# Optimization experiments

Hardware: AMD Instinct MI355X
Metric: run time of the kernel (lower is better)

Reference implementation:

```python
import jax, jax.numpy as jnp
import numpy as np

N_NODES = 50000
N_EDGES = 800000
IN_DIM = 256
HIDDEN = 64
HEADS1 = 4
HEADS2 = 1
N_CLASSES = 64
NEG_SLOPE = 0.2


def setup_inputs() -> dict:
    key = jax.random.key(0)
    ks = jax.random.split(key, 12)
    x = jax.random.normal(ks[0], (N_NODES, IN_DIM), dtype=jnp.float32)
    src = jax.random.randint(ks[1], (N_EDGES,), 0, N_NODES, dtype=jnp.int32)
    dst = jax.random.randint(ks[2], (N_EDGES,), 0, N_NODES, dtype=jnp.int32)
    s1 = 1.0 / np.sqrt(IN_DIM)
    s2 = 1.0 / np.sqrt(HIDDEN * HEADS1)
    W1 = jax.random.normal(ks[3], (IN_DIM, HEADS1 * HIDDEN), dtype=jnp.float32) * s1
    aL1 = jax.random.normal(ks[4], (HEADS1, HIDDEN), dtype=jnp.float32) * 0.1
    aR1 = jax.random.normal(ks[5], (HEADS1, HIDDEN), dtype=jnp.float32) * 0.1
    b1 = jnp.zeros((HEADS1 * HIDDEN,), dtype=jnp.float32)
    W2 = jax.random.normal(ks[6], (HEADS1 * HIDDEN, HEADS2 * N_CLASSES), dtype=jnp.float32) * s2
    aL2 = jax.random.normal(ks[7], (HEADS2, N_CLASSES), dtype=jnp.float32) * 0.1
    aR2 = jax.random.normal(ks[8], (HEADS2, N_CLASSES), dtype=jnp.float32) * 0.1
    b2 = jnp.zeros((HEADS2 * N_CLASSES,), dtype=jnp.float32)
    resW2 = jax.random.normal(ks[9], (HEADS1 * HIDDEN, HEADS2 * N_CLASSES), dtype=jnp.float32) * s2
    return {"x": x, "W1": W1, "aL1": aL1, "aR1": aR1, "b1": b1,
            "W2": W2, "aL2": aL2, "aR2": aR2, "b2": b2, "resW2": resW2,
            "src": src, "dst": dst}


def _gat_layer(h, W, aL, aR, b, src, dst, heads, out_dim, res_W=None, activation=None):
    n = h.shape[0]
    feat = (h @ W).reshape(n, heads, out_dim)          # [N, H, D]
    el = jnp.sum(feat * aL, axis=-1)                    # [N, H]
    er = jnp.sum(feat * aR, axis=-1)                    # [N, H]
    e = el[src] + er[dst]                               # [E, H]
    e = jnp.where(e > 0, e, NEG_SLOPE * e)              # leaky_relu
    # edge softmax over incoming edges of each destination node
    m = jax.ops.segment_max(e, dst, num_segments=n)
    ex = jnp.exp(e - m[dst])
    s = jax.ops.segment_sum(ex, dst, num_segments=n)
    sd = s[dst]
    a = ex / jnp.where(sd > 0, sd, 1.0)                 # [E, H]
    msg = feat[src] * a[:, :, None]                     # [E, H, D]
    rst = jax.ops.segment_sum(msg, dst, num_segments=n)  # [N, H, D]
    if res_W is not None:
        rst = rst + (h @ res_W).reshape(n, heads, out_dim)
    rst = rst + b.reshape(1, heads, out_dim)
    if activation is not None:
        rst = activation(rst)
    return rst


def reference(x, W1, aL1, aR1, b1, W2, aL2, aR2, b2, resW2, src, dst):
    h = _gat_layer(x, W1, aL1, aR1, b1, src, dst, HEADS1, HIDDEN,
                   res_W=None, activation=jax.nn.elu)
    h = h.reshape(N_NODES, HEADS1 * HIDDEN)             # flatten(1)
    h = _gat_layer(h, W2, aL2, aR2, b2, src, dst, HEADS2, N_CLASSES,
                   res_W=resW2, activation=None)
    return h.mean(axis=1)                               # mean over heads
```

## Files before the change

### kernel.cpp

```cpp
#include <hip/hip_runtime.h>
#include <hip/hip_bf16.h>
#include <math.h>

#define N_NODES 50000
#define N_EDGES 800000
#define IN_DIM  256
#define HID     64
#define H1      4
#define F1      256
#define NC      64
#define CHUNK   128
#define NB_SCAN 49

typedef __attribute__((ext_vector_type(8))) short short8v;
typedef __attribute__((ext_vector_type(4))) float float4v;

__device__ __forceinline__ float bf2f(unsigned short u){
  union { unsigned int i; float f; } c; c.i = ((unsigned int)u) << 16; return c.f;
}


__global__ __launch_bounds__(256) void prep_kernel(int* __restrict__ counts,
                                                   const float* __restrict__ W1,
                                                   const float* __restrict__ W2,
                                                   const float* __restrict__ resW2,
                                                   __hip_bfloat16* __restrict__ W1T,
                                                   __hip_bfloat16* __restrict__ B2T){
  int i = blockIdx.x*256 + threadIdx.x;
  if (i < N_NODES) counts[i] = 0;
  if (i < 256*256){
    int n = i >> 8, k = i & 255;
    W1T[n*256 + k] = __float2bfloat16(W1[k*256 + n]);
  }
  if (i < 128*256){
    int n = i >> 8, k = i & 255;
    float v = (n < 64) ? W2[k*64 + n] : resW2[k*64 + (n - 64)];
    B2T[n*256 + k] = __float2bfloat16(v);
  }
}


__global__ void hist_kernel(const int* __restrict__ dst, int* __restrict__ counts, int E4){
  int e4 = blockIdx.x*256 + threadIdx.x;
  if (e4 < E4){
    int4 d = ((const int4*)dst)[e4];
    atomicAdd(&counts[d.x], 1);
    atomicAdd(&counts[d.y], 1);
    atomicAdd(&counts[d.z], 1);
    atomicAdd(&counts[d.w], 1);
  }
}

__global__ __launch_bounds__(1024) void scan1_kernel(const int* __restrict__ counts,
                                                     int* __restrict__ part,
                                                     int* __restrict__ bsum, int n){
  __shared__ int wsum[16];
  int b = blockIdx.x, tid = threadIdx.x;
  int i = b*1024 + tid;
  int lane = tid & 63, wid = tid >> 6;
  int x = (i < n) ? counts[i] : 0;
  #pragma unroll
  for (int off = 1; off < 64; off <<= 1){ int t = __shfl_up(x, off); if (lane >= off) x += t; }
  if (lane == 63) wsum[wid] = x;
  __syncthreads();
  if (wid == 0 && lane < 16){
    int w = wsum[lane];
    #pragma unroll
    for (int off = 1; off < 16; off <<= 1){ int t = __shfl_up(w, off); if (lane >= off) w += t; }
    wsum[lane] = w;
  }
  __syncthreads();
  int incl = x + (wid ? wsum[wid-1] : 0);
  if (i < n) part[i] = incl;
  if (tid == 1023) bsum[b] = incl;
}

__global__ __launch_bounds__(1024) void scan3_kernel(const int* __restrict__ part,
                                                     const int* __restrict__ bsum,
                                                     int* __restrict__ row_ptr,
                                                     int* __restrict__ cursor, int n){
  __shared__ int off_s;
  int b = blockIdx.x, tid = threadIdx.x;
  if (tid < 64){
    int orig = (tid < NB_SCAN) ? bsum[tid] : 0;
    int x = orig;
    #pragma unroll
    for (int o = 1; o < 64; o <<= 1){ int t = __shfl_up(x, o); if (tid >= o) x += t; }
    if (tid == b) off_s = x - orig;
  }
  __syncthreads();
  int i = b*1024 + tid;
  if (i < n){
    int v = part[i] + off_s;
    row_ptr[i+1] = v; cursor[i+1] = v;
  }
  if (i == 0){ row_ptr[0] = 0; cursor[0] = 0; }
}

__global__ void fill_kernel(const int* __restrict__ src, const int* __restrict__ dst,
                            int* __restrict__ cursor, int* __restrict__ csr_src, int E){
  int e = blockIdx.x*256 + threadIdx.x;
  if (e < E){
    int slot = atomicAdd(&cursor[dst[e]], 1);
    csr_src[slot] = src[e];
  }
}


template<int LAYER, bool AFP32>
__device__ __forceinline__ void gemm_body(
    const void* __restrict__ Araw,
    const __hip_bfloat16* __restrict__ BT,
    __hip_bfloat16* __restrict__ Fb,
    float* __restrict__ Res,
    float* __restrict__ el, float* __restrict__ er,
    const float* __restrict__ aL, const float* __restrict__ aR,
    int M, int bm, int bn)
{
  constexpr int K = 256;
  __shared__ __hip_bfloat16 As[128*72];
  __shared__ __hip_bfloat16 Bs[128*72];
  int tid = threadIdx.x;
  int lane = tid & 63, w = tid >> 6;
  int wr = w >> 1, wc = w & 1;
  int l15 = lane & 15, l4 = lane >> 4;

  float4v acc[4][4];
  #pragma unroll
  for (int i=0;i<4;i++)
    #pragma unroll
    for (int j=0;j<4;j++) acc[i][j] = (float4v){0.f,0.f,0.f,0.f};

  for (int kt = 0; kt < K; kt += 64){
    #pragma unroll
    for (int it = 0; it < 4; it++){
      int chunk = tid + it*256;
      int r = chunk >> 3, kc = (chunk & 7)*8;
      int arow = bm*128 + r;
      if (AFP32){
        const float* Af = (const float*)Araw;
        float4 v0 = make_float4(0,0,0,0), v1 = make_float4(0,0,0,0);
        if (arow < M){
          v0 = *(const float4*)&Af[(size_t)arow*K + kt + kc];
          v1 = *(const float4*)&Af[(size_t)arow*K + kt + kc + 4];
        }
        __hip_bfloat16 t[8] = {__float2bfloat16(v0.x),__float2bfloat16(v0.y),
                               __float2bfloat16(v0.z),__float2bfloat16(v0.w),
                               __float2bfloat16(v1.x),__float2bfloat16(v1.y),
                               __float2bfloat16(v1.z),__float2bfloat16(v1.w)};
        *(int4*)&As[r*72 + kc] = *(int4*)t;
      } else {
        const __hip_bfloat16* Ab = (const __hip_bfloat16*)Araw;
        int4 va = make_int4(0,0,0,0);
        if (arow < M) va = *(const int4*)&Ab[(size_t)arow*K + kt + kc];
        *(int4*)&As[r*72 + kc] = va;
      }
      int brow = bn*128 + r;
      int4 vb = *(const int4*)&BT[(size_t)brow*K + kt + kc];
      *(int4*)&Bs[r*72 + kc] = vb;
    }
    __syncthreads();
    short8v af[4][2], bfr[4][2];
    #pragma unroll
    for (int mi=0;mi<4;mi++)
      #pragma unroll
      for (int kf=0;kf<2;kf++)
        af[mi][kf] = *(const short8v*)&As[(wr*64 + mi*16 + l15)*72 + kf*32 + l4*8];
    #pragma unroll
    for (int ni=0;ni<4;ni++)
      #pragma unroll
      for (int kf=0;kf<2;kf++)
        bfr[ni][kf] = *(const short8v*)&Bs[(wc*64 + ni*16 + l15)*72 + kf*32 + l4*8];
    #pragma unroll
    for (int mi=0;mi<4;mi++)
      #pragma unroll
      for (int ni=0;ni<4;ni++){
        acc[mi][ni] = __builtin_amdgcn_mfma_f32_16x16x32_bf16(af[mi][0], bfr[ni][0], acc[mi][ni], 0,0,0);
        acc[mi][ni] = __builtin_amdgcn_mfma_f32_16x16x32_bf16(af[mi][1], bfr[ni][1], acc[mi][ni], 0,0,0);
      }
    __syncthreads();
  }

  if (LAYER == 1){
    int h = bn*2 + wc;
    float aLv[4], aRv[4];
    #pragma unroll
    for (int ni=0;ni<4;ni++){ aLv[ni] = aL[h*64 + ni*16 + l15]; aRv[ni] = aR[h*64 + ni*16 + l15]; }
    #pragma unroll
    for (int mi=0;mi<4;mi++){
      #pragma unroll
      for (int r=0;r<4;r++){
        int row = bm*128 + wr*64 + mi*16 + l4*4 + r;
        float sl = 0.f, sr = 0.f;
        #pragma unroll
        for (int ni=0;ni<4;ni++){ float v = acc[mi][ni][r]; sl += v*aLv[ni]; sr += v*aRv[ni]; }
        #pragma unroll
        for (int off=1; off<16; off<<=1){ sl += __shfl_xor(sl, off); sr += __shfl_xor(sr, off); }
        if (row < M){
          #pragma unroll
          for (int ni=0;ni<4;ni++)
            Fb[(size_t)row*256 + h*64 + ni*16 + l15] = __float2bfloat16(acc[mi][ni][r]);
          if (l15 == 0){ el[row*4 + h] = sl; er[row*4 + h] = sr; }
        }
      }
    }
  } else {
    if (wc == 0){
      float aLv[4], aRv[4];
      #pragma unroll
      for (int ni=0;ni<4;ni++){ aLv[ni] = aL[ni*16 + l15]; aRv[ni] = aR[ni*16 + l15]; }
      #pragma unroll
      for (int mi=0;mi<4;mi++){
        #pragma unroll
        for (int r=0;r<4;r++){
          int row = bm*128 + wr*64 + mi*16 + l4*4 + r;
          float sl = 0.f, sr = 0.f;
          #pragma unroll
          for (int ni=0;ni<4;ni++){ float v = acc[mi][ni][r]; sl += v*aLv[ni]; sr += v*aRv[ni]; }
          #pragma unroll
          for (int off=1; off<16; off<<=1){ sl += __shfl_xor(sl, off); sr += __shfl_xor(sr, off); }
          if (row < M){
            #pragma unroll
            for (int ni=0;ni<4;ni++)
              Fb[(size_t)row*64 + ni*16 + l15] = __float2bfloat16(acc[mi][ni][r]);
            if (l15 == 0){ el[row] = sl; er[row] = sr; }
          }
        }
      }
    } else {
      #pragma unroll
      for (int mi=0;mi<4;mi++){
        #pragma unroll
        for (int r=0;r<4;r++){
          int row = bm*128 + wr*64 + mi*16 + l4*4 + r;
          if (row < M){
            #pragma unroll
            for (int ni=0;ni<4;ni++)
              Res[(size_t)row*64 + ni*16 + l15] = acc[mi][ni][r];
          }
        }
      }
    }
  }
}

__global__ __launch_bounds__(256) void gemm1_kernel(
    const float* __restrict__ x, const __hip_bfloat16* __restrict__ W1T,
    __hip_bfloat16* __restrict__ featb,
    float* __restrict__ el, float* __restrict__ er,
    const float* __restrict__ aL, const float* __restrict__ aR)
{
  int id = blockIdx.x;
  int bn = (id >> 3) & 1;
  int bm = (id & 7) | ((id >> 4) << 3);
  if (bm*128 >= N_NODES) return;
  gemm_body<1,true>(x, W1T, featb, nullptr, el, er, aL, aR, N_NODES, bm, bn);
}

__global__ __launch_bounds__(256) void gemm2_kernel(
    const __hip_bfloat16* __restrict__ A, const __hip_bfloat16* __restrict__ BT,
    __hip_bfloat16* __restrict__ Fb, float* __restrict__ Res,
    float* __restrict__ el, float* __restrict__ er,
    const float* __restrict__ aL, const float* __restrict__ aR, int M)
{
  gemm_body<2,false>(A, BT, Fb, Res, el, er, aL, aR, M, blockIdx.x, 0);
}


__global__ __launch_bounds__(256) void agg1_kernel(const int* __restrict__ row_ptr,
                                                   const int* __restrict__ csr_src,
                                                   const float* __restrict__ el,
                                                   const float* __restrict__ er,
                                                   const __hip_bfloat16* __restrict__ featb,
                                                   const float* __restrict__ bias,
                                                   __hip_bfloat16* __restrict__ h1b, int N){
  __shared__ int   ssh[4][CHUNK];
  __shared__ float wsh[4][CHUNK][4];
  int lane = threadIdx.x & 63, wv = threadIdx.x >> 6;
  int n = blockIdx.x*4 + wv;
  if (n >= N) return;
  int rs = row_ptr[n], re = row_ptr[n+1];
  int half = lane >> 5;
  int l31 = lane & 31;
  int hl = l31 >> 3;
  float4 ern4 = *(const float4*)&er[(size_t)n*4];
  float ernv[4] = {ern4.x, ern4.y, ern4.z, ern4.w};
  float acc[8] = {0.f,0.f,0.f,0.f,0.f,0.f,0.f,0.f};
  float ssum4[4] = {0.f,0.f,0.f,0.f};

  for (int base = rs; base < re; base += CHUNK){
    int cnt = min(CHUNK, re - base);
    int padded = (cnt + 7) & ~7;
    for (int t = lane; t < padded; t += 64){
      float w4[4] = {0.f,0.f,0.f,0.f};
      int s = 0;
      if (t < cnt){
        s = csr_src[base + t];
        float4 e4 = *(const float4*)&el[(size_t)s*4];
        float ev[4] = {e4.x, e4.y, e4.z, e4.w};
        #pragma unroll
        for (int h = 0; h < 4; h++){
          float e = ev[h] + ernv[h];
          e = e > 0.f ? e : 0.2f*e;
          float ex = __expf(e);
          w4[h] = ex;
          ssum4[h] += ex;
        }
      }
      ssh[wv][t] = s;
      *(float4*)&wsh[wv][t][0] = make_float4(w4[0], w4[1], w4[2], w4[3]);
    }
    for (int jb = 0; jb < padded; jb += 8){
      int t0 = jb + half, t1 = jb + 2 + half, t2 = jb + 4 + half, t3 = jb + 6 + half;
      int s0 = ssh[wv][t0], s1 = ssh[wv][t1], s2 = ssh[wv][t2], s3 = ssh[wv][t3];
      float w0 = wsh[wv][t0][hl], w1 = wsh[wv][t1][hl];
      float w2 = wsh[wv][t2][hl], w3 = wsh[wv][t3][hl];
      short8v f0 = *(const short8v*)&featb[(size_t)s0*256 + l31*8];
      short8v f1 = *(const short8v*)&featb[(size_t)s1*256 + l31*8];
      short8v f2 = *(const short8v*)&featb[(size_t)s2*256 + l31*8];
      short8v f3 = *(const short8v*)&featb[(size_t)s3*256 + l31*8];
      #pragma unroll
      for (int q = 0; q < 8; q++){
        acc[q] += w0 * bf2f((unsigned short)f0[q]);
        acc[q] += w1 * bf2f((unsigned short)f1[q]);
        acc[q] += w2 * bf2f((unsigned short)f2[q]);
        acc[q] += w3 * bf2f((unsigned short)f3[q]);
      }
    }
  }
  #pragma unroll
  for (int off = 32; off; off >>= 1)
    #pragma unroll
    for (int h = 0; h < 4; h++) ssum4[h] += __shfl_xor(ssum4[h], off);
  #pragma unroll
  for (int q = 0; q < 8; q++) acc[q] += __shfl_xor(acc[q], 32);
  float inv = ssum4[hl] > 0.f ? 1.f/ssum4[hl] : 0.f;
  if (lane < 32){
    float4 b0 = *(const float4*)&bias[l31*8];
    float4 b1v = *(const float4*)&bias[l31*8 + 4];
    float bb[8] = {b0.x,b0.y,b0.z,b0.w,b1v.x,b1v.y,b1v.z,b1v.w};
    __hip_bfloat16 o[8];
    #pragma unroll
    for (int q = 0; q < 8; q++){
      float v = acc[q]*inv + bb[q];
      v = v > 0.f ? v : __expf(v) - 1.f;
      o[q] = __float2bfloat16(v);
    }
    *(short8v*)&h1b[(size_t)n*256 + l31*8] = *(short8v*)o;
  }
}

__global__ __launch_bounds__(256) void agg2_kernel(const int* __restrict__ row_ptr,
                                                   const int* __restrict__ csr_src,
                                                   const float* __restrict__ el,
                                                   const float* __restrict__ er,
                                                   const __hip_bfloat16* __restrict__ f2b,
                                                   const float* __restrict__ res,
                                                   const float* __restrict__ bias,
                                                   float* __restrict__ out, int N){
  __shared__ int   ssh[4][CHUNK];
  __shared__ float wsh[4][CHUNK];
  int lane = threadIdx.x & 63, wv = threadIdx.x >> 6;
  int n = blockIdx.x*4 + wv;
  if (n >= N) return;
  int rs = row_ptr[n], re = row_ptr[n+1];
  int q4 = lane >> 4;
  int l15 = lane & 15;
  float ern = er[n];
  float acc[4] = {0.f,0.f,0.f,0.f};
  float ssum = 0.f;

  for (int base = rs; base < re; base += CHUNK){
    int cnt = min(CHUNK, re - base);
    int padded = (cnt + 15) & ~15;
    for (int t = lane; t < padded; t += 64){
      float w = 0.f; int s = 0;
      if (t < cnt){
        s = csr_src[base + t];
        float e = el[s] + ern;
        e = e > 0.f ? e : 0.2f*e;
        w = __expf(e);
        ssum += w;
      }
      ssh[wv][t] = s;
      wsh[wv][t] = w;
    }
    for (int jb = 0; jb < padded; jb += 16){
      int t0 = jb + q4, t1 = jb + 4 + q4, t2 = jb + 8 + q4, t3 = jb + 12 + q4;
      int s0 = ssh[wv][t0], s1 = ssh[wv][t1], s2 = ssh[wv][t2], s3 = ssh[wv][t3];
      float w0 = wsh[wv][t0], w1 = wsh[wv][t1], w2 = wsh[wv][t2], w3 = wsh[wv][t3];
      ushort4 f0 = *(const ushort4*)&f2b[(size_t)s0*NC + l15*4];
      ushort4 f1 = *(const ushort4*)&f2b[(size_t)s1*NC + l15*4];
      ushort4 f2 = *(const ushort4*)&f2b[(size_t)s2*NC + l15*4];
      ushort4 f3 = *(const ushort4*)&f2b[(size_t)s3*NC + l15*4];
      acc[0] += w0*bf2f(f0.x) + w1*bf2f(f1.x) + w2*bf2f(f2.x) + w3*bf2f(f3.x);
      acc[1] += w0*bf2f(f0.y) + w1*bf2f(f1.y) + w2*bf2f(f2.y) + w3*bf2f(f3.y);
      acc[2] += w0*bf2f(f0.z) + w1*bf2f(f1.z) + w2*bf2f(f2.z) + w3*bf2f(f3.z);
      acc[3] += w0*bf2f(f0.w) + w1*bf2f(f1.w) + w2*bf2f(f2.w) + w3*bf2f(f3.w);
    }
  }
  #pragma unroll
  for (int off = 32; off; off >>= 1) ssum += __shfl_xor(ssum, off);
  #pragma unroll
  for (int q = 0; q < 4; q++){
    acc[q] += __shfl_xor(acc[q], 16);
    acc[q] += __shfl_xor(acc[q], 32);
  }
  float inv = ssum > 0.f ? 1.f/ssum : 0.f;
  if (lane < 16){
    float4 r4 = *(const float4*)&res[(size_t)n*NC + l15*4];
    float4 b4 = *(const float4*)&bias[l15*4];
    float4 o;
    o.x = acc[0]*inv + r4.x + b4.x;
    o.y = acc[1]*inv + r4.y + b4.y;
    o.z = acc[2]*inv + r4.z + b4.z;
    o.w = acc[3]*inv + r4.w + b4.w;
    *(float4*)&out[(size_t)n*NC + l15*4] = o;
  }
}


extern "C" void kernel_launch(void* const* d_in, const int* in_sizes, int n_in,
                              void* d_out, int out_size, void* d_ws, size_t ws_size,
                              hipStream_t stream){
  const float* x     = (const float*)d_in[0];
  const float* W1    = (const float*)d_in[1];
  const float* aL1   = (const float*)d_in[2];
  const float* aR1   = (const float*)d_in[3];
  const float* b1    = (const float*)d_in[4];
  const float* W2    = (const float*)d_in[5];
  const float* aL2   = (const float*)d_in[6];
  const float* aR2   = (const float*)d_in[7];
  const float* b2    = (const float*)d_in[8];
  const float* resW2 = (const float*)d_in[9];
  const int*   src   = (const int*)d_in[10];
  const int*   dst   = (const int*)d_in[11];
  float* out = (float*)d_out;

  char* p = (char*)d_ws;
  auto alloc = [&](size_t bytes)->void*{
    void* r = (void*)p; p += (bytes + 255) & ~(size_t)255; return r;
  };
  __hip_bfloat16* featb = (__hip_bfloat16*)alloc((size_t)N_NODES*F1*2);
  __hip_bfloat16* h1b   = (__hip_bfloat16*)alloc((size_t)N_NODES*F1*2);
  __hip_bfloat16* f2b   = (__hip_bfloat16*)alloc((size_t)N_NODES*NC*2);
  float* res   = (float*)alloc((size_t)N_NODES*NC*4);
  float* el1   = (float*)alloc((size_t)N_NODES*H1*4);
  float* er1   = (float*)alloc((size_t)N_NODES*H1*4);
  float* el2   = (float*)alloc((size_t)N_NODES*4);
  float* er2   = (float*)alloc((size_t)N_NODES*4);
  int* counts  = (int*)alloc((size_t)N_NODES*4);
  int* part    = (int*)alloc((size_t)N_NODES*4);
  int* bsum    = (int*)alloc((size_t)64*4);
  int* row_ptr = (int*)alloc((size_t)(N_NODES+1)*4);
  int* cursor  = (int*)alloc((size_t)(N_NODES+1)*4);
  int* csr_src = (int*)alloc((size_t)N_EDGES*4);
  __hip_bfloat16* W1T = (__hip_bfloat16*)alloc((size_t)256*256*2);
  __hip_bfloat16* B2T = (__hip_bfloat16*)alloc((size_t)128*256*2);

  int nb = (N_NODES + 1023)/1024;
  prep_kernel<<<256, 256, 0, stream>>>(counts, W1, W2, resW2, W1T, B2T);
  hist_kernel<<<(N_EDGES/4+255)/256, 256, 0, stream>>>(dst, counts, N_EDGES/4);
  scan1_kernel<<<nb, 1024, 0, stream>>>(counts, part, bsum, N_NODES);
  scan3_kernel<<<nb, 1024, 0, stream>>>(part, bsum, row_ptr, cursor, N_NODES);
  fill_kernel<<<(N_EDGES+255)/256, 256, 0, stream>>>(src, dst, cursor, csr_src, N_EDGES);

  gemm1_kernel<<<800, 256, 0, stream>>>(x, W1T, featb, el1, er1, aL1, aR1);
  agg1_kernel<<<(N_NODES+3)/4, 256, 0, stream>>>(row_ptr, csr_src, el1, er1, featb, b1, h1b, N_NODES);

  gemm2_kernel<<<(N_NODES+127)/128, 256, 0, stream>>>(h1b, B2T, f2b, res,
                                                      el2, er2, aL2, aR2, N_NODES);
  agg2_kernel<<<(N_NODES+3)/4, 256, 0, stream>>>(row_ptr, csr_src, el2, er2, f2b, res, b2, out, N_NODES);
}
```

Before: 234.5 us.

## Fuse CSR fill into gemm1 launch and histogram into weight prep kernel

Merges independent kernels by splitting the block range of a single launch: the dst histogram shares a launch with the weight transpose and cast, and the CSR fill shares a launch with the layer-1 GEMM. Zeroing of counts moves to a memset. The aim is fewer launches and letting the atomic-bound fill overlap with the compute-bound GEMM on otherwise idle CUs. In exchange, the fill blocks contend with GEMM blocks for memory bandwidth and scheduling slots, and the added memset is an extra queued operation.

```diff
diff --git a/kernel.cpp b/kernel.cpp
--- a/kernel.cpp
+++ b/kernel.cpp
@@ -11,6 +11,9 @@
 #define NC      64
 #define CHUNK   128
 #define NB_SCAN 49
+#define GEMM1_BLOCKS 800
+#define FILL_BLOCKS  ((N_EDGES+255)/256)
+#define HIST4_BLOCKS ((N_EDGES/4+255)/256)
 
 typedef __attribute__((ext_vector_type(8))) short short8v;
 typedef __attribute__((ext_vector_type(4))) float float4v;
@@ -20,36 +23,35 @@
 }
 
 
-__global__ __launch_bounds__(256) void prep_kernel(int* __restrict__ counts,
-                                                   const float* __restrict__ W1,
-                                                   const float* __restrict__ W2,
-                                                   const float* __restrict__ resW2,
-                                                   __hip_bfloat16* __restrict__ W1T,
-                                                   __hip_bfloat16* __restrict__ B2T){
-  int i = blockIdx.x*256 + threadIdx.x;
-  if (i < N_NODES) counts[i] = 0;
-  if (i < 256*256){
-    int n = i >> 8, k = i & 255;
-    W1T[n*256 + k] = __float2bfloat16(W1[k*256 + n]);
-  }
-  if (i < 128*256){
-    int n = i >> 8, k = i & 255;
-    float v = (n < 64) ? W2[k*64 + n] : resW2[k*64 + (n - 64)];
-    B2T[n*256 + k] = __float2bfloat16(v);
-  }
-}
-
-
-__global__ void hist_kernel(const int* __restrict__ dst, int* __restrict__ counts, int E4){
-  int e4 = blockIdx.x*256 + threadIdx.x;
-  if (e4 < E4){
-    int4 d = ((const int4*)dst)[e4];
-    atomicAdd(&counts[d.x], 1);
-    atomicAdd(&counts[d.y], 1);
-    atomicAdd(&counts[d.z], 1);
-    atomicAdd(&counts[d.w], 1);
-  }
-}
+__global__ __launch_bounds__(256) void hist_prepw_kernel(
+    const int* __restrict__ dst, int* __restrict__ counts,
+    const float* __restrict__ W1, const float* __restrict__ W2,
+    const float* __restrict__ resW2,
+    __hip_bfloat16* __restrict__ W1T, __hip_bfloat16* __restrict__ B2T){
+  int b = blockIdx.x;
+  if (b < HIST4_BLOCKS){
+    int e4 = b*256 + threadIdx.x;
+    if (e4 < N_EDGES/4){
+      int4 d = ((const int4*)dst)[e4];
+      atomicAdd(&counts[d.x], 1);
+      atomicAdd(&counts[d.y], 1);
+      atomicAdd(&counts[d.z], 1);
+      atomicAdd(&counts[d.w], 1);
+    }
+  } else {
+    int i = (b - HIST4_BLOCKS)*256 + threadIdx.x;
+    if (i < 256*256){
+      int n = i >> 8, k = i & 255;
+      W1T[n*256 + k] = __float2bfloat16(W1[k*256 + n]);
+    } else if (i < 256*256 + 128*256){
+      int j = i - 256*256;
+      int n = j >> 8, k = j & 255;
+      float v = (n < 64) ? W2[k*64 + n] : resW2[k*64 + (n - 64)];
+      B2T[n*256 + k] = __float2bfloat16(v);
+    }
+  }
+}
+
 
 __global__ __launch_bounds__(1024) void scan1_kernel(const int* __restrict__ counts,
                                                      int* __restrict__ part,
@@ -95,15 +97,6 @@
     row_ptr[i+1] = v; cursor[i+1] = v;
   }
   if (i == 0){ row_ptr[0] = 0; cursor[0] = 0; }
-}
-
-__global__ void fill_kernel(const int* __restrict__ src, const int* __restrict__ dst,
-                            int* __restrict__ cursor, int* __restrict__ csr_src, int E){
-  int e = blockIdx.x*256 + threadIdx.x;
-  if (e < E){
-    int slot = atomicAdd(&cursor[dst[e]], 1);
-    csr_src[slot] = src[e];
-  }
 }
 
 
@@ -244,17 +237,27 @@
   }
 }
 
-__global__ __launch_bounds__(256) void gemm1_kernel(
+__global__ __launch_bounds__(256) void gemm1_fill_kernel(
     const float* __restrict__ x, const __hip_bfloat16* __restrict__ W1T,
     __hip_bfloat16* __restrict__ featb,
     float* __restrict__ el, float* __restrict__ er,
-    const float* __restrict__ aL, const float* __restrict__ aR)
+    const float* __restrict__ aL, const float* __restrict__ aR,
+    const int* __restrict__ src, const int* __restrict__ dst,
+    int* __restrict__ cursor, int* __restrict__ csr_src)
 {
   int id = blockIdx.x;
-  int bn = (id >> 3) & 1;
-  int bm = (id & 7) | ((id >> 4) << 3);
-  if (bm*128 >= N_NODES) return;
-  gemm_body<1,true>(x, W1T, featb, nullptr, el, er, aL, aR, N_NODES, bm, bn);
+  if (id < GEMM1_BLOCKS){
+    int bn = (id >> 3) & 1;
+    int bm = (id & 7) | ((id >> 4) << 3);
+    if (bm*128 >= N_NODES) return;
+    gemm_body<1,true>(x, W1T, featb, nullptr, el, er, aL, aR, N_NODES, bm, bn);
+  } else {
+    int e = (id - GEMM1_BLOCKS)*256 + threadIdx.x;
+    if (e < N_EDGES){
+      int slot = atomicAdd(&cursor[dst[e]], 1);
+      csr_src[slot] = src[e];
+    }
+  }
 }
 
 __global__ __launch_bounds__(256) void gemm2_kernel(
@@ -459,13 +462,16 @@
   __hip_bfloat16* B2T = (__hip_bfloat16*)alloc((size_t)128*256*2);
 
   int nb = (N_NODES + 1023)/1024;
-  prep_kernel<<<256, 256, 0, stream>>>(counts, W1, W2, resW2, W1T, B2T);
-  hist_kernel<<<(N_EDGES/4+255)/256, 256, 0, stream>>>(dst, counts, N_EDGES/4);
+  int prepw_blocks = (256*256 + 128*256 + 255)/256;
+  hipMemsetAsync(counts, 0, (size_t)N_NODES*4, stream);
+  hist_prepw_kernel<<<HIST4_BLOCKS + prepw_blocks, 256, 0, stream>>>(dst, counts,
+                                                                     W1, W2, resW2, W1T, B2T);
   scan1_kernel<<<nb, 1024, 0, stream>>>(counts, part, bsum, N_NODES);
   scan3_kernel<<<nb, 1024, 0, stream>>>(part, bsum, row_ptr, cursor, N_NODES);
-  fill_kernel<<<(N_EDGES+255)/256, 256, 0, stream>>>(src, dst, cursor, csr_src, N_EDGES);
-
-  gemm1_kernel<<<800, 256, 0, stream>>>(x, W1T, featb, el1, er1, aL1, aR1);
+
+  gemm1_fill_kernel<<<GEMM1_BLOCKS + FILL_BLOCKS, 256, 0, stream>>>(
+      x, W1T, featb, el1, er1, aL1, aR1, src, dst, cursor, csr_src);
+
   agg1_kernel<<<(N_NODES+3)/4, 256, 0, stream>>>(row_ptr, csr_src, el1, er1, featb, b1, h1b, N_NODES);
 
   gemm2_kernel<<<(N_NODES+127)/128, 256, 0, stream>>>(h1b, B2T, f2b, res,
```

New measurement: 210.3 us. 1.11x faster.
